# Kernel tuning notes

Measured on AMD Instinct MI355X. Metric: run time of the kernel, lower is better.

The kernel has to match this reference:

```python
import jax, jax.numpy as jnp
import numpy as np

HIDDEN = 1024
HEAD_SIZE = 16
HEAD_DIM = HIDDEN // HEAD_SIZE
EPS = 1e-6
N = 65536


def setup_inputs() -> dict:
    key = jax.random.key(0)
    ks = jax.random.split(key, 10)
    s = 1.0 / np.sqrt(HIDDEN)
    return {
        "x": jax.random.normal(ks[0], (N, HIDDEN), jnp.float32),
        "y": jax.random.normal(ks[1], (N, HIDDEN), jnp.float32),
        "x_replica": jax.random.randint(ks[2], (N,), 0, N),
        "ln_w": jnp.ones((HIDDEN,), jnp.float32),
        "q_w": jax.random.uniform(ks[3], (HIDDEN, HIDDEN), jnp.float32, -s, s),
        "q_b": jax.random.uniform(ks[4], (HIDDEN,), jnp.float32, -s, s),
        "k_w": jax.random.uniform(ks[5], (HIDDEN, HIDDEN), jnp.float32, -s, s),
        "k_b": jax.random.uniform(ks[6], (HIDDEN,), jnp.float32, -s, s),
        "v_w": jax.random.uniform(ks[7], (HIDDEN, HIDDEN), jnp.float32, -s, s),
        "v_b": jax.random.uniform(ks[8], (HIDDEN,), jnp.float32, -s, s),
    }


def _rmsnorm(x, w):
    var = jnp.mean(x * x, axis=-1, keepdims=True)
    return w * (x * jax.lax.rsqrt(var + EPS))


def reference(x, y, x_replica, ln_w, q_w, q_b, k_w, k_b, v_w, v_b):
    h = _rmsnorm(x, ln_w)
    x_q = h @ q_w.T + q_b                      # [N, H]
    x_q = x_q[x_replica]                       # gather rows -> [N, H]
    y_k = y @ k_w.T + k_b                      # [N, H]
    q = x_q.reshape(-1, HEAD_DIM)              # [N*heads, d]
    k = y_k.reshape(-1, HEAD_DIM)
    dot = jnp.sum(q * k, axis=-1)
    qn = jnp.maximum(jnp.linalg.norm(q, axis=-1), EPS)
    kn = jnp.maximum(jnp.linalg.norm(k, axis=-1), EPS)
    att = (dot / (qn * kn)).reshape(-1, HEAD_SIZE, 1)  # [N, heads, 1]
    v = (y @ v_w.T + v_b).reshape(-1, HEAD_SIZE, HEAD_DIM)
    v = (v * att).reshape(x_q.shape)
    return x + v
```

## Files before the change

kernel.cpp:

```cpp
#include <hip/hip_runtime.h>


typedef unsigned short u16;
typedef unsigned int u32;
typedef __attribute__((ext_vector_type(4))) unsigned short u16x4;
typedef __attribute__((ext_vector_type(8))) short short8;
typedef __attribute__((ext_vector_type(4))) float floatx4;

#define NROW 65536
#define HID  1024

__device__ __forceinline__ u16 f2bf(float f) {
  union { float f; u32 u; } v; v.f = f;
  u32 r = v.u + 0x7fffu + ((v.u >> 16) & 1u);
  return (u16)(r >> 16);
}
__device__ __forceinline__ float bf2f(u32 hbits) {
  union { u32 u; float f; } v; v.u = hbits << 16;
  return v.f;
}

__device__ __forceinline__ void gl_lds16(const void* g, void* l) {
  __builtin_amdgcn_global_load_lds(
      (const __attribute__((address_space(1))) void*)g,
      (__attribute__((address_space(3))) void*)l,
      16, 0, 0);
}

__global__ void __launch_bounds__(256) cast_bf16_kernel(
    const float* __restrict__ in, u16* __restrict__ out, int n4) {
  int i = blockIdx.x * 256 + threadIdx.x;
  if (i < n4) {
    float4 v = ((const float4*)in)[i];
    u16x4 o;
    o.x = f2bf(v.x); o.y = f2bf(v.y); o.z = f2bf(v.z); o.w = f2bf(v.w);
    ((u16x4*)out)[i] = o;
  }
}

__global__ void __launch_bounds__(256) rmsnorm_cast_kernel(
    const float* __restrict__ x, const float* __restrict__ w, u16* __restrict__ h) {
  const int row = blockIdx.x;
  const int tid = threadIdx.x;
  const float4 v = ((const float4*)(x + (size_t)row * HID))[tid];
  float ss = v.x * v.x + v.y * v.y + v.z * v.z + v.w * v.w;
  #pragma unroll
  for (int m = 32; m >= 1; m >>= 1) ss += __shfl_xor(ss, m);
  __shared__ float sbuf[4];
  if ((tid & 63) == 0) sbuf[tid >> 6] = ss;
  __syncthreads();
  const float tot = sbuf[0] + sbuf[1] + sbuf[2] + sbuf[3];
  const float sc = rsqrtf(tot * (1.0f / HID) + 1e-6f);
  const float4 wv = ((const float4*)w)[tid];
  u16x4 o;
  o.x = f2bf(v.x * wv.x * sc);
  o.y = f2bf(v.y * wv.y * sc);
  o.z = f2bf(v.z * wv.z * sc);
  o.w = f2bf(v.w * wv.w * sc);
  ((u16x4*)(h + (size_t)row * HID))[tid] = o;
}

__global__ void __launch_bounds__(256) gemm_kernel(
    const u16* __restrict__ A, const u16* __restrict__ W,
    const float* __restrict__ bias,
    u16* __restrict__ out_bf,
    const float* __restrict__ att, const float* __restrict__ xres,
    float* __restrict__ out_f, int mode) {
  __shared__ u16 As[128 * 64];
  __shared__ u16 Bs[128 * 64];

  const int tid  = threadIdx.x;
  const int wid  = tid >> 6;
  const int lane = tid & 63;
  const int l15  = lane & 15;
  const int quad = lane >> 4;
  const int rowBase = blockIdx.y * 128;
  const int colBase = blockIdx.x * 128;
  const int wm = (wid >> 1) * 64;
  const int wn = (wid & 1) * 64;

  floatx4 acc[4][4];
  #pragma unroll
  for (int i = 0; i < 4; i++)
    #pragma unroll
    for (int j = 0; j < 4; j++) acc[i][j] = (floatx4){0.f, 0.f, 0.f, 0.f};

  for (int k0 = 0; k0 < HID; k0 += 64) {
    __syncthreads();
    #pragma unroll
    for (int t = 0; t < 4; t++) {
      const int e = wid * 2048 + t * 512 + lane * 8;
      const int r = e >> 6, c = e & 63;
      gl_lds16(A + (size_t)(rowBase + r) * HID + (k0 + c), &As[wid * 2048 + t * 512]);
      gl_lds16(W + (size_t)(colBase + r) * HID + (k0 + c), &Bs[wid * 2048 + t * 512]);
    }
    __syncthreads();
    #pragma unroll
    for (int kk = 0; kk < 64; kk += 32) {
      short8 af[4], bfr[4];
      #pragma unroll
      for (int mt = 0; mt < 4; mt++)
        af[mt] = *(const short8*)&As[(wm + mt * 16 + l15) * 64 + kk + quad * 8];
      #pragma unroll
      for (int nt = 0; nt < 4; nt++)
        bfr[nt] = *(const short8*)&Bs[(wn + nt * 16 + l15) * 64 + kk + quad * 8];
      #pragma unroll
      for (int mt = 0; mt < 4; mt++)
        #pragma unroll
        for (int nt = 0; nt < 4; nt++)
          acc[mt][nt] = __builtin_amdgcn_mfma_f32_16x16x32_bf16(
              af[mt], bfr[nt], acc[mt][nt], 0, 0, 0);
    }
  }

  #pragma unroll
  for (int nt = 0; nt < 4; nt++) {
    const int col = colBase + wn + nt * 16 + l15;
    const float b = bias[col];
    #pragma unroll
    for (int mt = 0; mt < 4; mt++) {
      #pragma unroll
      for (int r = 0; r < 4; r++) {
        const int row = rowBase + wm + mt * 16 + quad * 4 + r;
        const float v = acc[mt][nt][r] + b;
        const size_t idx = (size_t)row * HID + col;
        if (mode == 0) {
          out_bf[idx] = f2bf(v);
        } else {
          const float a = att[(size_t)row * 16 + (col >> 6)];
          out_f[idx] = xres[idx] + v * a;
        }
      }
    }
  }
}

__global__ void __launch_bounds__(64) att_kernel(
    const u16* __restrict__ xq, const u16* __restrict__ yk,
    const int* __restrict__ rep, float* __restrict__ att) {
  const int n = blockIdx.x;
  const int lane = threadIdx.x;
  const u16* q = xq + (size_t)rep[n] * HID + lane * 16;
  const u16* k = yk + (size_t)n * HID + lane * 16;
  float dot = 0.f, qq = 0.f, kk = 0.f;
  #pragma unroll
  for (int j = 0; j < 2; j++) {
    const uint4 qv = ((const uint4*)q)[j];
    const uint4 kv = ((const uint4*)k)[j];
    const u32 qa[4] = {qv.x, qv.y, qv.z, qv.w};
    const u32 ka[4] = {kv.x, kv.y, kv.z, kv.w};
    #pragma unroll
    for (int i = 0; i < 4; i++) {
      const float a0 = bf2f(qa[i] & 0xffffu), a1 = bf2f(qa[i] >> 16);
      const float b0 = bf2f(ka[i] & 0xffffu), b1 = bf2f(ka[i] >> 16);
      dot += a0 * b0 + a1 * b1;
      qq  += a0 * a0 + a1 * a1;
      kk  += b0 * b0 + b1 * b1;
    }
  }
  dot += __shfl_xor(dot, 1); dot += __shfl_xor(dot, 2);
  qq  += __shfl_xor(qq, 1);  qq  += __shfl_xor(qq, 2);
  kk  += __shfl_xor(kk, 1);  kk  += __shfl_xor(kk, 2);
  if ((lane & 3) == 0) {
    const float qn = fmaxf(sqrtf(qq), 1e-6f);
    const float kn = fmaxf(sqrtf(kk), 1e-6f);
    att[(size_t)n * 16 + (lane >> 2)] = dot / (qn * kn);
  }
}

extern "C" void kernel_launch(void* const* d_in, const int* in_sizes, int n_in,
                              void* d_out, int out_size, void* d_ws, size_t ws_size,
                              hipStream_t stream) {
  const float* x   = (const float*)d_in[0];
  const float* y   = (const float*)d_in[1];
  const int*   rep = (const int*)d_in[2];
  const float* lnw = (const float*)d_in[3];
  const float* qw  = (const float*)d_in[4];
  const float* qb  = (const float*)d_in[5];
  const float* kw  = (const float*)d_in[6];
  const float* kb  = (const float*)d_in[7];
  const float* vw  = (const float*)d_in[8];
  const float* vb  = (const float*)d_in[9];
  float* out = (float*)d_out;

  const size_t NH = (size_t)NROW * HID;
  const size_t WW = (size_t)HID * HID;

  u16*  y_bf  = (u16*)d_ws;
  u16*  hk_bf = y_bf + NH;
  u16*  w_q   = hk_bf + NH;
  u16*  w_k   = w_q + WW;
  u16*  w_v   = w_k + WW;
  float* att  = (float*)(w_v + WW);
  const size_t base_need = (2 * NH + 3 * WW) * sizeof(u16) + (size_t)NROW * 16 * sizeof(float);
  u16* xq_bf;
  if (ws_size >= base_need + NH * sizeof(u16))
    xq_bf = (u16*)(att + (size_t)NROW * 16);
  else
    xq_bf = (u16*)d_out;

  cast_bf16_kernel<<<(int)(WW / 4 / 256), 256, 0, stream>>>(qw, w_q, (int)(WW / 4));
  cast_bf16_kernel<<<(int)(WW / 4 / 256), 256, 0, stream>>>(kw, w_k, (int)(WW / 4));
  cast_bf16_kernel<<<(int)(WW / 4 / 256), 256, 0, stream>>>(vw, w_v, (int)(WW / 4));
  cast_bf16_kernel<<<(int)(NH / 4 / 256), 256, 0, stream>>>(y, y_bf, (int)(NH / 4));
  rmsnorm_cast_kernel<<<NROW, 256, 0, stream>>>(x, lnw, hk_bf);

  dim3 grid(HID / 128, NROW / 128), block(256);
  gemm_kernel<<<grid, block, 0, stream>>>(hk_bf, w_q, qb, xq_bf, nullptr, nullptr, nullptr, 0);
  gemm_kernel<<<grid, block, 0, stream>>>(y_bf, w_k, kb, hk_bf, nullptr, nullptr, nullptr, 0);
  att_kernel<<<NROW, 64, 0, stream>>>(xq_bf, hk_bf, rep, att);
  gemm_kernel<<<grid, block, 0, stream>>>(y_bf, w_v, vb, nullptr, att, x, out, 1);
}
```

Measured before the change: 1.622 ms.

## Double-buffer GEMM LDS tiles with XOR swizzle and XCD-aware block remap

The GEMM main loop now keeps two LDS buffers and prefetches the next K-slice with global_load_lds while MFMAs run on the current one. Explicit vmcnt waits and barriers replace the two syncthreads per iteration. LDS columns are XOR-swizzled by row to cut bank conflicts on the fragment reads. Block indices are remapped so each XCD works on a contiguous band of rows, which should improve L2 reuse of the A tiles. The cost is double the LDS use, which may lower occupancy, and hand-managed waitcnt synchronisation that is easy to get wrong.

Measured after the change: 1.537 ms. -5.2%, faster.

```diff
diff --git a/kernel.cpp b/kernel.cpp
--- a/kernel.cpp
+++ b/kernel.cpp
@@ -66,16 +66,21 @@
     u16* __restrict__ out_bf,
     const float* __restrict__ att, const float* __restrict__ xres,
     float* __restrict__ out_f, int mode) {
-  __shared__ u16 As[128 * 64];
-  __shared__ u16 Bs[128 * 64];
+  __shared__ u16 As[2][128 * 64];
+  __shared__ u16 Bs[2][128 * 64];
 
   const int tid  = threadIdx.x;
   const int wid  = tid >> 6;
   const int lane = tid & 63;
   const int l15  = lane & 15;
   const int quad = lane >> 4;
-  const int rowBase = blockIdx.y * 128;
-  const int colBase = blockIdx.x * 128;
+
+  const int L    = blockIdx.y * 8 + blockIdx.x;
+  const int xcd  = L & 7;
+  const int j    = L >> 3;
+  const int rowBase = (xcd * 64 + (j >> 3)) * 128;
+  const int colBase = (j & 7) * 128;
+
   const int wm = (wid >> 1) * 64;
   const int wn = (wid & 1) * 64;
 
@@ -83,27 +88,48 @@
   #pragma unroll
   for (int i = 0; i < 4; i++)
     #pragma unroll
-    for (int j = 0; j < 4; j++) acc[i][j] = (floatx4){0.f, 0.f, 0.f, 0.f};
-
-  for (int k0 = 0; k0 < HID; k0 += 64) {
-    __syncthreads();
-    #pragma unroll
-    for (int t = 0; t < 4; t++) {
-      const int e = wid * 2048 + t * 512 + lane * 8;
-      const int r = e >> 6, c = e & 63;
-      gl_lds16(A + (size_t)(rowBase + r) * HID + (k0 + c), &As[wid * 2048 + t * 512]);
-      gl_lds16(W + (size_t)(colBase + r) * HID + (k0 + c), &Bs[wid * 2048 + t * 512]);
-    }
-    __syncthreads();
+    for (int jj = 0; jj < 4; jj++) acc[i][jj] = (floatx4){0.f, 0.f, 0.f, 0.f};
+
+  #define STAGE(b, k0)                                                        \
+    {                                                                         \
+      _Pragma("unroll")                                                       \
+      for (int t = 0; t < 4; t++) {                                           \
+        const int e = wid * 2048 + t * 512 + lane * 8;                        \
+        const int r = e >> 6;                                                 \
+        const int c = (e & 63) ^ ((r & 7) << 3);     \
+        gl_lds16(A + (size_t)(rowBase + r) * HID + ((k0) + c),                \
+                 &As[b][wid * 2048 + t * 512]);                               \
+        gl_lds16(W + (size_t)(colBase + r) * HID + ((k0) + c),                \
+                 &Bs[b][wid * 2048 + t * 512]);                               \
+      }                                                                       \
+    }
+
+  STAGE(0, 0);
+  int cur = 0;
+  const int swz = (l15 & 7) << 3;
+
+  for (int it = 0; it < 16; ++it) {
+    if (it < 15) {
+      STAGE(cur ^ 1, (it + 1) * 64);
+      asm volatile("s_waitcnt vmcnt(8)" ::: "memory");
+    } else {
+      asm volatile("s_waitcnt vmcnt(0)" ::: "memory");
+    }
+    __builtin_amdgcn_sched_barrier(0);
+    __builtin_amdgcn_s_barrier();
+
+    const u16* as = As[cur];
+    const u16* bs = Bs[cur];
     #pragma unroll
     for (int kk = 0; kk < 64; kk += 32) {
       short8 af[4], bfr[4];
+      const int cidx = (kk + quad * 8) ^ swz;
       #pragma unroll
       for (int mt = 0; mt < 4; mt++)
-        af[mt] = *(const short8*)&As[(wm + mt * 16 + l15) * 64 + kk + quad * 8];
+        af[mt] = *(const short8*)&as[(wm + mt * 16 + l15) * 64 + cidx];
       #pragma unroll
       for (int nt = 0; nt < 4; nt++)
-        bfr[nt] = *(const short8*)&Bs[(wn + nt * 16 + l15) * 64 + kk + quad * 8];
+        bfr[nt] = *(const short8*)&bs[(wn + nt * 16 + l15) * 64 + cidx];
       #pragma unroll
       for (int mt = 0; mt < 4; mt++)
         #pragma unroll
@@ -111,7 +137,10 @@
           acc[mt][nt] = __builtin_amdgcn_mfma_f32_16x16x32_bf16(
               af[mt], bfr[nt], acc[mt][nt], 0, 0, 0);
     }
-  }
+    __builtin_amdgcn_s_barrier();
+    cur ^= 1;
+  }
+  #undef STAGE
 
   #pragma unroll
   for (int nt = 0; nt < 4; nt++) {
```
